# Optimization experiments

Hardware: AMD Instinct MI355X
Metric: run time of the kernel (lower is better)

The kernel has to match this reference:

```python
import jax, jax.numpy as jnp
import numpy as np

N = 100000
E = 1600000
H = 128
L = 3


def setup_inputs() -> dict:
    key = jax.random.key(0)
    ks = jax.random.split(key, 8)
    z = jax.random.normal(ks[0], (N, H), dtype=jnp.float32)
    edge_index = jax.random.randint(ks[1], (2, E), 0, N, dtype=jnp.int64)
    edge_weight = jax.random.uniform(ks[2], (E,), dtype=jnp.float32)
    s = 1.0 / np.sqrt(H)
    weight = jax.random.uniform(ks[3], (L, H, H), minval=-s, maxval=s, dtype=jnp.float32)
    w_ih = jax.random.uniform(ks[4], (3 * H, H), minval=-s, maxval=s, dtype=jnp.float32)
    w_hh = jax.random.uniform(ks[5], (3 * H, H), minval=-s, maxval=s, dtype=jnp.float32)
    b_ih = jax.random.uniform(ks[6], (3 * H,), minval=-s, maxval=s, dtype=jnp.float32)
    b_hh = jax.random.uniform(ks[7], (3 * H,), minval=-s, maxval=s, dtype=jnp.float32)
    return {"z": z, "edge_weight": edge_weight, "weight": weight,
            "w_ih": w_ih, "w_hh": w_hh, "b_ih": b_ih, "b_hh": b_hh,
            "edge_index": edge_index}


def _gru_cell(m, h, w_ih, w_hh, b_ih, b_hh):
    # torch GRUCell: gate order (r, z, n)
    gi = m @ w_ih.T + b_ih   # [N, 3H]
    gh = h @ w_hh.T + b_hh   # [N, 3H]
    i_r, i_z, i_n = jnp.split(gi, 3, axis=-1)
    h_r, h_z, h_n = jnp.split(gh, 3, axis=-1)
    r = jax.nn.sigmoid(i_r + h_r)
    zg = jax.nn.sigmoid(i_z + h_z)
    n = jnp.tanh(i_n + r * h_n)
    return (1.0 - zg) * n + zg * h


def reference(z, edge_weight, weight, w_ih, w_hh, b_ih, b_hh, edge_index):
    src = edge_index[0]  # x_j gathered from source nodes
    dst = edge_index[1]  # aggregated at target nodes
    x = z  # in_channels == out_channels, so no zero padding needed
    for l in range(L):
        m = x @ weight[l]                                  # [N, H]
        msg = m[src] * edge_weight[:, None]                # [E, H]
        agg = jax.ops.segment_sum(msg, dst, num_segments=N)  # aggr='add'
        x = _gru_cell(agg, x, w_ih, w_hh, b_ih, b_hh)
    return x
```

## Files before the change

kernel.cpp:

```cpp
#include <hip/hip_runtime.h>

typedef __bf16 bf16x8 __attribute__((ext_vector_type(8)));
typedef float floatx4 __attribute__((ext_vector_type(4)));

#define NPB 256
#define NPB_SHIFT 8
#define MAXNB 1024
#define TILE 4096

static __device__ __forceinline__ float bfu_to_f(unsigned short u) {
    unsigned int x = ((unsigned int)u) << 16;
    return __builtin_bit_cast(float, x);
}
static __device__ __forceinline__ unsigned short f_to_bfu(float f) {
    unsigned int u = __builtin_bit_cast(unsigned int, f);
    unsigned int r = (u + 0x7fffu + ((u >> 16) & 1u)) >> 16;
    return (unsigned short)r;
}

__global__ void detect_k(const unsigned short* __restrict__ bih_u,
                         const unsigned int* __restrict__ ei_u,
                         int* __restrict__ flags) {
    __shared__ int sv, sz;
    int t = threadIdx.x;
    if (t == 0) { sv = 0; sz = 0; }
    __syncthreads();
    unsigned short u = bih_u[2 * t];
    unsigned int ex = (u >> 7) & 0xFF;
    if (ex >= 64 && ex < 124) atomicAdd(&sv, 1);
    if (ei_u[2 * t + 1] == 0u) atomicAdd(&sz, 1);
    __syncthreads();
    if (t == 0) {
        flags[0] = (sv >= 48) ? 1 : 0;
        flags[1] = (sz == 64) ? 1 : 0;
    }
}


__global__ void cvt_bf16_k(const void* __restrict__ in, unsigned short* __restrict__ out,
                           int n, const int* __restrict__ flags) {
    int i = blockIdx.x * 256 + threadIdx.x;
    if (i >= n) return;
    if (flags[0]) out[i] = ((const unsigned short*)in)[i];
    else out[i] = f_to_bfu(((const float*)in)[i]);
}

__global__ void cvt_bias_k(const void* __restrict__ bih, const void* __restrict__ bhh,
                           float* __restrict__ bih_f, float* __restrict__ bhh_f,
                           const int* __restrict__ flags) {
    int i = blockIdx.x * 256 + threadIdx.x;
    if (i >= 768) return;
    const void* src = (i < 384) ? bih : bhh;
    int j = (i < 384) ? i : i - 384;
    float v = flags[0] ? bfu_to_f(((const unsigned short*)src)[j]) : ((const float*)src)[j];
    if (i < 384) bih_f[j] = v;
    else bhh_f[j] = v;
}


static __device__ __forceinline__ int load_idx(const unsigned int* eiu, size_t pos, int is64) {
    return (int)eiu[is64 ? 2 * pos : pos];
}

__global__ __launch_bounds__(256) void count_k(const unsigned int* __restrict__ eiu,
                                               int* __restrict__ bucketCnt, int E,
                                               const int* __restrict__ flags) {
    __shared__ int cnt[MAXNB];
    int t = threadIdx.x;
    for (int b = t; b < MAXNB; b += 256) cnt[b] = 0;
    __syncthreads();
    int is64 = flags[1];
    int e0 = blockIdx.x * TILE;
    int e1 = min(e0 + TILE, E);
    for (int e = e0 + t; e < e1; e += 256) {
        int d = load_idx(eiu, (size_t)E + e, is64);
        atomicAdd(&cnt[d >> NPB_SHIFT], 1);
    }
    __syncthreads();
    for (int b = t; b < MAXNB; b += 256) {
        int c = cnt[b];
        if (c) atomicAdd(&bucketCnt[b], c);
    }
}

__global__ void scanB_k(const int* __restrict__ bucketCnt, int* __restrict__ bucketBase,
                        int* __restrict__ bucketCursor, int NB, int E) {
    __shared__ int sh[MAXNB];
    int t = threadIdx.x;
    int v = (t < NB) ? bucketCnt[t] : 0;
    sh[t] = v;
    __syncthreads();
    for (int off = 1; off < MAXNB; off <<= 1) {
        int u = (t >= off) ? sh[t - off] : 0;
        __syncthreads();
        sh[t] += u;
        __syncthreads();
    }
    if (t < NB) {
        int b = sh[t] - v;
        bucketBase[t] = b;
        bucketCursor[t] = b;
    }
    if (t == 0) bucketBase[NB] = E;
}

__global__ __launch_bounds__(256) void bin_k(const unsigned int* __restrict__ eiu,
                                             const void* __restrict__ ew,
                                             int* __restrict__ bucketCursor,
                                             uint2* __restrict__ rec8, int E,
                                             const int* __restrict__ flags) {
    __shared__ int cnt[MAXNB];
    __shared__ int basel[MAXNB];
    int t = threadIdx.x;
    for (int b = t; b < MAXNB; b += 256) cnt[b] = 0;
    __syncthreads();
    int is64 = flags[1];
    int isb = flags[0];
    int e0 = blockIdx.x * TILE;
    int e1 = min(e0 + TILE, E);
    for (int e = e0 + t; e < e1; e += 256) {
        int d = load_idx(eiu, (size_t)E + e, is64);
        atomicAdd(&cnt[d >> NPB_SHIFT], 1);
    }
    __syncthreads();
    for (int b = t; b < MAXNB; b += 256) {
        int c = cnt[b];
        basel[b] = c ? atomicAdd(&bucketCursor[b], c) : 0;
        cnt[b] = 0;
    }
    __syncthreads();
    for (int e = e0 + t; e < e1; e += 256) {
        int s = load_idx(eiu, (size_t)e, is64);
        int d = load_idx(eiu, (size_t)E + e, is64);
        float w = isb ? bfu_to_f(((const unsigned short*)ew)[e]) : ((const float*)ew)[e];
        int b = d >> NPB_SHIFT;
        int p = basel[b] + atomicAdd(&cnt[b], 1);
        rec8[p] = make_uint2((unsigned int)s | ((unsigned int)(d & 255) << 20),
                             __builtin_bit_cast(unsigned int, w));
    }
}

__global__ __launch_bounds__(256) void csr_k(const uint2* __restrict__ rec8,
                                             const int* __restrict__ bucketBase,
                                             int* __restrict__ offsets,
                                             uint2* __restrict__ rec, int N, int E) {
    __shared__ int cnt[NPB];
    __shared__ int sh[NPB];
    __shared__ int cur[NPB];
    int t = threadIdx.x;
    int b = blockIdx.x;
    int n0 = b << NPB_SHIFT;
    int nodes = min(NPB, N - n0);
    int ebase = bucketBase[b];
    int ecnt = bucketBase[b + 1] - ebase;

    cnt[t] = 0;
    __syncthreads();
    for (int i = t; i < ecnt; i += 256) {
        int d = (rec8[ebase + i].x >> 20) & 255;
        atomicAdd(&cnt[d], 1);
    }
    __syncthreads();
    int v = cnt[t];
    sh[t] = v;
    __syncthreads();
    for (int off = 1; off < NPB; off <<= 1) {
        int u = (t >= off) ? sh[t - off] : 0;
        __syncthreads();
        sh[t] += u;
        __syncthreads();
    }
    int loff = sh[t] - v;
    if (t < nodes) offsets[n0 + t] = ebase + loff;
    cur[t] = ebase + loff;
    if (b == 0 && t == 0) offsets[N] = E;
    __syncthreads();
    for (int i = t; i < ecnt; i += 256) {
        uint2 r = rec8[ebase + i];
        int d = (r.x >> 20) & 255;
        int p = atomicAdd(&cur[d], 1);
        rec[p] = make_uint2(r.x & 0xFFFFFu, r.y);
    }
}


static __device__ __forceinline__ float dot8_bf(uint4 wv, uint4 iv) {
    float s;
    s  = bfu_to_f((unsigned short)(wv.x)) * bfu_to_f((unsigned short)(iv.x));
    s += bfu_to_f((unsigned short)(wv.x >> 16)) * bfu_to_f((unsigned short)(iv.x >> 16));
    s += bfu_to_f((unsigned short)(wv.y)) * bfu_to_f((unsigned short)(iv.y));
    s += bfu_to_f((unsigned short)(wv.y >> 16)) * bfu_to_f((unsigned short)(iv.y >> 16));
    s += bfu_to_f((unsigned short)(wv.z)) * bfu_to_f((unsigned short)(iv.z));
    s += bfu_to_f((unsigned short)(wv.z >> 16)) * bfu_to_f((unsigned short)(iv.z >> 16));
    s += bfu_to_f((unsigned short)(wv.w)) * bfu_to_f((unsigned short)(iv.w));
    s += bfu_to_f((unsigned short)(wv.w >> 16)) * bfu_to_f((unsigned short)(iv.w >> 16));
    return s;
}

__global__ void make_ut_k(const void* __restrict__ weight, const void* __restrict__ wih,
                          unsigned short* __restrict__ Ut, const int* __restrict__ flags) {
    int idx = blockIdx.x * 256 + threadIdx.x;
    if (idx >= 3 * 384 * 128) return;
    int isb = flags[0];
    int a = idx & 127;
    int j = (idx >> 7) % 384;
    int l = idx / (384 * 128);
    float s = 0.f;
    if (isb) {
        const uint4* W4 = (const uint4*)((const unsigned short*)weight + (size_t)l * 16384 + a * 128);
        const uint4* I4 = (const uint4*)((const unsigned short*)wih + (size_t)j * 128);
#pragma unroll
        for (int c = 0; c < 16; c++) s += dot8_bf(W4[c], I4[c]);
    } else {
        const float4* W4 = (const float4*)((const float*)weight + (size_t)l * 16384 + a * 128);
        const float4* I4 = (const float4*)((const float*)wih + (size_t)j * 128);
#pragma unroll
        for (int c = 0; c < 32; c++) {
            float4 w = W4[c], i = I4[c];
            s += w.x * i.x + w.y * i.y + w.z * i.z + w.w * i.w;
        }
    }
    Ut[idx] = f_to_bfu(s);
}

__global__ void pack_b_k(const unsigned short* __restrict__ Ut,
                         const void* __restrict__ whh,
                         unsigned short* __restrict__ Bp,
                         const int* __restrict__ flags) {
    int idx = blockIdx.x * 256 + threadIdx.x;
    if (idx >= 3 * 4 * 12 * 4 * 64) return;
    int lane = idx & 63;
    int kc = (idx >> 6) & 3;
    int rest = idx >> 8;
    int j = rest % 12;
    int cg = (rest / 12) & 3;
    int l = rest / 48;
    int s = j / 6;
    int g = (j % 6) >> 1;
    int t = j & 1;
    int col = (cg * 2 + t) * 16 + (lane & 15);
    int k = kc * 32 + (lane >> 4) * 8;
    int row384 = g * 128 + col;
    unsigned short tmp[8];
    const unsigned short* src;
    if (s == 0) {
        src = Ut + (size_t)l * 49152 + row384 * 128 + k;
    } else if (flags[0]) {
        src = (const unsigned short*)whh + (size_t)row384 * 128 + k;
    } else {
        const float* wf = (const float*)whh + (size_t)row384 * 128 + k;
        for (int i = 0; i < 8; i++) tmp[i] = f_to_bfu(wf[i]);
        src = tmp;
    }
    unsigned short* dst = Bp + (size_t)l * 98304 + (((size_t)(cg * 12 + j) * 4 + kc) * 64 + lane) * 8;
    for (int i = 0; i < 8; i++) dst[i] = src[i];
}


__global__ __launch_bounds__(256) void agg_k(const unsigned short* __restrict__ xb,
                                             const int* __restrict__ offs,
                                             const uint2* __restrict__ rec,
                                             unsigned short* __restrict__ y, int N,
                                             int nch) {
    int bid = blockIdx.x;
    int c = ((bid & 7) << 3) + ((bid >> 3) & 7) + ((bid >> 6) << 6);
    if (c >= nch) return;
    int node = c * 16 + (threadIdx.x >> 4);
    int l16 = threadIdx.x & 15;
    if (node >= N) return;
    int b = offs[node];
    int e2 = offs[node + 1];
    const uint4* xp4 = (const uint4*)xb;
    float a0[8], a1[8];
#pragma unroll
    for (int i = 0; i < 8; i++) { a0[i] = 0.f; a1[i] = 0.f; }

    auto fma_row = [&](float* acc, uint4 v, float w) {
        acc[0] += w * __builtin_bit_cast(float, v.x << 16);
        acc[1] += w * __builtin_bit_cast(float, v.x & 0xffff0000u);
        acc[2] += w * __builtin_bit_cast(float, v.y << 16);
        acc[3] += w * __builtin_bit_cast(float, v.y & 0xffff0000u);
        acc[4] += w * __builtin_bit_cast(float, v.z << 16);
        acc[5] += w * __builtin_bit_cast(float, v.z & 0xffff0000u);
        acc[6] += w * __builtin_bit_cast(float, v.w << 16);
        acc[7] += w * __builtin_bit_cast(float, v.w & 0xffff0000u);
    };

    int e = b;
    for (; e + 4 <= e2; e += 4) {
        uint2 r0 = rec[e], r1 = rec[e + 1], r2 = rec[e + 2], r3 = rec[e + 3];
        uint4 v0 = xp4[(size_t)r0.x * 16 + l16];
        uint4 v1 = xp4[(size_t)r1.x * 16 + l16];
        uint4 v2 = xp4[(size_t)r2.x * 16 + l16];
        uint4 v3 = xp4[(size_t)r3.x * 16 + l16];
        fma_row(a0, v0, __builtin_bit_cast(float, r0.y));
        fma_row(a1, v1, __builtin_bit_cast(float, r1.y));
        fma_row(a0, v2, __builtin_bit_cast(float, r2.y));
        fma_row(a1, v3, __builtin_bit_cast(float, r3.y));
    }
    for (; e < e2; e++) {
        uint2 r = rec[e];
        uint4 v = xp4[(size_t)r.x * 16 + l16];
        fma_row(a0, v, __builtin_bit_cast(float, r.y));
    }

    uint4 o;
    o.x = (unsigned int)f_to_bfu(a0[0] + a1[0]) | ((unsigned int)f_to_bfu(a0[1] + a1[1]) << 16);
    o.y = (unsigned int)f_to_bfu(a0[2] + a1[2]) | ((unsigned int)f_to_bfu(a0[3] + a1[3]) << 16);
    o.z = (unsigned int)f_to_bfu(a0[4] + a1[4]) | ((unsigned int)f_to_bfu(a0[5] + a1[5]) << 16);
    o.w = (unsigned int)f_to_bfu(a0[6] + a1[6]) | ((unsigned int)f_to_bfu(a0[7] + a1[7]) << 16);
    ((uint4*)y)[(size_t)node * 16 + l16] = o;
}


__global__ __launch_bounds__(512, 4) void gru_k(const unsigned short* __restrict__ y,
                                                const unsigned short* __restrict__ xin,
                                                void* __restrict__ xout,
                                                const unsigned short* __restrict__ Bp,
                                                const float* __restrict__ bih,
                                                const float* __restrict__ bhh, int N,
                                                const int* __restrict__ flags, int last) {
    __shared__ uint4 Blds[3072];

    int bid = blockIdx.x;
    int r8 = bid & 7;
    int inner = bid >> 3;
    int cg = inner & 3;
    int rb = ((inner >> 2) << 3) + r8;
    int row0 = rb << 7;
    if (row0 >= N) return;

    int tid = threadIdx.x;
    {
        const uint4* bsrc = (const uint4*)(Bp + (size_t)cg * 24576);
#pragma unroll
        for (int i = 0; i < 6; i++) Blds[tid + i * 512] = bsrc[tid + i * 512];
    }
    __syncthreads();

    int wave = tid >> 6;
    int wc = wave & 1;
    int wr = wave >> 1;
    int lane = tid & 63;
    int quad = lane >> 4;
    int m16 = lane & 15;
    const unsigned short* bl = (const unsigned short*)Blds;

    int rA[2];
#pragma unroll
    for (int rt = 0; rt < 2; rt++) {
        int r = row0 + wr * 32 + rt * 16 + m16;
        rA[rt] = (r < N) ? r : N - 1;
    }

    floatx4 acc[2][4];
#pragma unroll
    for (int rt = 0; rt < 2; rt++)
#pragma unroll
        for (int s = 0; s < 4; s++) acc[rt][s] = (floatx4){0.f, 0.f, 0.f, 0.f};

    bf16x8 aY[2][4], aX[2][4];

#pragma unroll
    for (int rt = 0; rt < 2; rt++)
#pragma unroll
        for (int kc = 0; kc < 4; kc++)
            aY[rt][kc] = *(const bf16x8*)(y + (size_t)rA[rt] * 128 + kc * 32 + quad * 8);
    __builtin_amdgcn_sched_barrier(0);

#pragma unroll
    for (int rt = 0; rt < 2; rt++)
#pragma unroll
        for (int kc = 0; kc < 4; kc++)
            aX[rt][kc] = *(const bf16x8*)(xin + (size_t)rA[rt] * 128 + kc * 32 + quad * 8);

#pragma unroll
    for (int kc = 0; kc < 4; kc++) {
#pragma unroll
        for (int g = 0; g < 3; g++) {
            int jU = g * 2 + wc;
            bf16x8 b = *(const bf16x8*)(bl + ((size_t)(jU * 4 + kc) * 64 + lane) * 8);
            int s = (g == 2) ? 2 : g;
            acc[0][s] = __builtin_amdgcn_mfma_f32_16x16x32_bf16(aY[0][kc], b, acc[0][s], 0, 0, 0);
            acc[1][s] = __builtin_amdgcn_mfma_f32_16x16x32_bf16(aY[1][kc], b, acc[1][s], 0, 0, 0);
        }
    }
    __builtin_amdgcn_sched_barrier(0);

#pragma unroll
    for (int kc = 0; kc < 4; kc++) {
#pragma unroll
        for (int g = 0; g < 3; g++) {
            int jW = 6 + g * 2 + wc;
            bf16x8 b = *(const bf16x8*)(bl + ((size_t)(jW * 4 + kc) * 64 + lane) * 8);
            int s = (g == 2) ? 3 : g;
            acc[0][s] = __builtin_amdgcn_mfma_f32_16x16x32_bf16(aX[0][kc], b, acc[0][s], 0, 0, 0);
            acc[1][s] = __builtin_amdgcn_mfma_f32_16x16x32_bf16(aX[1][kc], b, acc[1][s], 0, 0, 0);
        }
    }

    int ch = cg * 32 + wc * 16 + m16;
    float b_r = bih[ch] + bhh[ch];
    float b_z = bih[128 + ch] + bhh[128 + ch];
    float bi_n = bih[256 + ch];
    float bh_n = bhh[256 + ch];
    int isb = last ? flags[0] : 1;
#pragma unroll
    for (int rt = 0; rt < 2; rt++) {
#pragma unroll
        for (int ri = 0; ri < 4; ri++) {
            int row = row0 + wr * 32 + rt * 16 + quad * 4 + ri;
            if (row >= N) continue;
            float sr = acc[rt][0][ri] + b_r;
            float sz = acc[rt][1][ri] + b_z;
            float gn = acc[rt][2][ri] + bi_n;
            float hn = acc[rt][3][ri] + bh_n;
            float r = __builtin_amdgcn_rcpf(1.f + __expf(-sr));
            float zg = __builtin_amdgcn_rcpf(1.f + __expf(-sz));
            float x2 = gn + r * hn;
            float n = 1.f - 2.f * __builtin_amdgcn_rcpf(1.f + __expf(2.f * x2));
            float h = bfu_to_f(xin[(size_t)row * 128 + ch]);
            float o = n + zg * (h - n);
            if (isb) ((unsigned short*)xout)[(size_t)row * 128 + ch] = f_to_bfu(o);
            else ((float*)xout)[(size_t)row * 128 + ch] = o;
        }
    }
}


extern "C" void kernel_launch(void* const* d_in, const int* in_sizes, int n_in,
                              void* d_out, int out_size, void* d_ws, size_t ws_size,
                              hipStream_t stream) {
    const int N = in_sizes[0] / 128;
    const int E = in_sizes[1];
    const int NB = (N + NPB - 1) >> NPB_SHIFT;

    const void* z = d_in[0];
    const void* ew = d_in[1];
    const void* weight = d_in[2];
    const void* wih = d_in[3];
    const void* whh = d_in[4];
    const void* bih = d_in[5];
    const void* bhh = d_in[6];
    const unsigned int* eiu = (const unsigned int*)d_in[7];

    unsigned short* y01 = (unsigned short*)d_out;

    size_t off = 0;
    char* base = (char*)d_ws;
    auto carve = [&](size_t bytes) -> void* {
        void* p = base + off;
        off = (off + bytes + 255) & ~(size_t)255;
        return p;
    };
    unsigned short* xb = (unsigned short*)carve((size_t)N * 128 * 2);
    unsigned short* xb2 = (unsigned short*)carve((size_t)N * 128 * 2);
    uint2* rec8 = (uint2*)carve((size_t)E * 8);
    uint2* rec = (uint2*)carve((size_t)E * 8);
    int* offsets = (int*)carve((size_t)(N + 1) * 4);
    int* bucketCnt = (int*)carve(MAXNB * 4);
    int* bucketBase = (int*)carve((MAXNB + 1) * 4);
    int* bucketCursor = (int*)carve(MAXNB * 4);
    unsigned short* Ut = (unsigned short*)carve((size_t)3 * 384 * 128 * 2);
    unsigned short* Bp = (unsigned short*)carve((size_t)3 * 48 * 4 * 64 * 8 * 2);
    float* bih_f = (float*)carve(384 * 4);
    float* bhh_f = (float*)carve(384 * 4);
    int* flags = (int*)carve(256);

    detect_k<<<1, 64, 0, stream>>>((const unsigned short*)bih, eiu, flags);

    cvt_bf16_k<<<(N * 128 + 255) / 256, 256, 0, stream>>>(z, xb, N * 128, flags);
    cvt_bias_k<<<3, 256, 0, stream>>>(bih, bhh, bih_f, bhh_f, flags);

    hipMemsetAsync(bucketCnt, 0, MAXNB * 4, stream);
    int gbin = (E + TILE - 1) / TILE;
    count_k<<<gbin, 256, 0, stream>>>(eiu, bucketCnt, E, flags);
    scanB_k<<<1, MAXNB, 0, stream>>>(bucketCnt, bucketBase, bucketCursor, NB, E);
    bin_k<<<gbin, 256, 0, stream>>>(eiu, ew, bucketCursor, rec8, E, flags);
    csr_k<<<NB, NPB, 0, stream>>>(rec8, bucketBase, offsets, rec, N, E);

    make_ut_k<<<(3 * 384 * 128 + 255) / 256, 256, 0, stream>>>(weight, wih, Ut, flags);
    pack_b_k<<<(3 * 4 * 12 * 4 * 64 + 255) / 256, 256, 0, stream>>>(Ut, whh, Bp, flags);

    const int RB = (N + 127) >> 7;
    const int grid_gru = 8 * ((RB + 7) >> 3) * 4;
    const int nch = (N + 15) >> 4;
    const int grid_agg = ((nch + 63) >> 6) << 6;

    agg_k<<<grid_agg, 256, 0, stream>>>(xb, offsets, rec, y01, N, nch);
    gru_k<<<grid_gru, 512, 0, stream>>>(y01, xb, xb2, Bp, bih_f, bhh_f, N, flags, 0);
    agg_k<<<grid_agg, 256, 0, stream>>>(xb2, offsets, rec, y01, N, nch);
    gru_k<<<grid_gru, 512, 0, stream>>>(y01, xb2, xb, Bp + 98304, bih_f, bhh_f, N, flags, 0);
    agg_k<<<grid_agg, 256, 0, stream>>>(xb, offsets, rec, xb2, N, nch);
    gru_k<<<grid_gru, 512, 0, stream>>>(xb2, xb, d_out, Bp + 2 * 98304, bih_f, bhh_f, N, flags, 1);
}
```

Before: 588.6 us.

## Shrink GRU tile to 16 output channels per block, doubling grid

Measured after the change: 577.8 us. About the same (-1.8%).

```diff
diff --git a/kernel.cpp b/kernel.cpp
--- a/kernel.cpp
+++ b/kernel.cpp
@@ -228,17 +228,16 @@
                          unsigned short* __restrict__ Bp,
                          const int* __restrict__ flags) {
     int idx = blockIdx.x * 256 + threadIdx.x;
-    if (idx >= 3 * 4 * 12 * 4 * 64) return;
+    if (idx >= 3 * 8 * 6 * 4 * 64) return;
     int lane = idx & 63;
     int kc = (idx >> 6) & 3;
     int rest = idx >> 8;
-    int j = rest % 12;
-    int cg = (rest / 12) & 3;
+    int j = rest % 6;
+    int cg8 = (rest / 6) & 7;
     int l = rest / 48;
-    int s = j / 6;
-    int g = (j % 6) >> 1;
-    int t = j & 1;
-    int col = (cg * 2 + t) * 16 + (lane & 15);
+    int s = j / 3;
+    int g = j % 3;
+    int col = cg8 * 16 + (lane & 15);
     int k = kc * 32 + (lane >> 4) * 8;
     int row384 = g * 128 + col;
     unsigned short tmp[8];
@@ -252,7 +251,7 @@
         for (int i = 0; i < 8; i++) tmp[i] = f_to_bfu(wf[i]);
         src = tmp;
     }
-    unsigned short* dst = Bp + (size_t)l * 98304 + (((size_t)(cg * 12 + j) * 4 + kc) * 64 + lane) * 8;
+    unsigned short* dst = Bp + (size_t)l * 98304 + (((size_t)(cg8 * 6 + j) * 4 + kc) * 64 + lane) * 8;
     for (int i = 0; i < 8; i++) dst[i] = src[i];
 }
 
@@ -313,76 +312,62 @@
 }
 
 
-__global__ __launch_bounds__(512, 4) void gru_k(const unsigned short* __restrict__ y,
+__global__ __launch_bounds__(512, 6) void gru_k(const unsigned short* __restrict__ y,
                                                 const unsigned short* __restrict__ xin,
                                                 void* __restrict__ xout,
                                                 const unsigned short* __restrict__ Bp,
                                                 const float* __restrict__ bih,
                                                 const float* __restrict__ bhh, int N,
                                                 const int* __restrict__ flags, int last) {
-    __shared__ uint4 Blds[3072];
+    __shared__ uint4 Blds[1536];
 
     int bid = blockIdx.x;
     int r8 = bid & 7;
     int inner = bid >> 3;
-    int cg = inner & 3;
-    int rb = ((inner >> 2) << 3) + r8;
+    int cg8 = inner & 7;
+    int rb = ((inner >> 3) << 3) + r8;
     int row0 = rb << 7;
     if (row0 >= N) return;
 
     int tid = threadIdx.x;
     {
-        const uint4* bsrc = (const uint4*)(Bp + (size_t)cg * 24576);
-#pragma unroll
-        for (int i = 0; i < 6; i++) Blds[tid + i * 512] = bsrc[tid + i * 512];
-    }
-    __syncthreads();
-
-    int wave = tid >> 6;
-    int wc = wave & 1;
-    int wr = wave >> 1;
+        const uint4* bsrc = (const uint4*)(Bp + (size_t)cg8 * 12288);
+#pragma unroll
+        for (int i = 0; i < 3; i++) Blds[tid + i * 512] = bsrc[tid + i * 512];
+    }
+    __syncthreads();
+
+    int wr = tid >> 6;
     int lane = tid & 63;
     int quad = lane >> 4;
     int m16 = lane & 15;
     const unsigned short* bl = (const unsigned short*)Blds;
 
-    int rA[2];
-#pragma unroll
-    for (int rt = 0; rt < 2; rt++) {
-        int r = row0 + wr * 32 + rt * 16 + m16;
-        rA[rt] = (r < N) ? r : N - 1;
-    }
-
-    floatx4 acc[2][4];
-#pragma unroll
-    for (int rt = 0; rt < 2; rt++)
-#pragma unroll
-        for (int s = 0; s < 4; s++) acc[rt][s] = (floatx4){0.f, 0.f, 0.f, 0.f};
-
-    bf16x8 aY[2][4], aX[2][4];
-
-#pragma unroll
-    for (int rt = 0; rt < 2; rt++)
-#pragma unroll
-        for (int kc = 0; kc < 4; kc++)
-            aY[rt][kc] = *(const bf16x8*)(y + (size_t)rA[rt] * 128 + kc * 32 + quad * 8);
+    int r = row0 + wr * 16 + m16;
+    int rA = (r < N) ? r : N - 1;
+
+    floatx4 acc[4];
+#pragma unroll
+    for (int s = 0; s < 4; s++) acc[s] = (floatx4){0.f, 0.f, 0.f, 0.f};
+
+    bf16x8 aY[4], aX[4];
+
+#pragma unroll
+    for (int kc = 0; kc < 4; kc++)
+        aY[kc] = *(const bf16x8*)(y + (size_t)rA * 128 + kc * 32 + quad * 8);
     __builtin_amdgcn_sched_barrier(0);
 
 #pragma unroll
-    for (int rt = 0; rt < 2; rt++)
-#pragma unroll
-        for (int kc = 0; kc < 4; kc++)
-            aX[rt][kc] = *(const bf16x8*)(xin + (size_t)rA[rt] * 128 + kc * 32 + quad * 8);
+    for (int kc = 0; kc < 4; kc++)
+        aX[kc] = *(const bf16x8*)(xin + (size_t)rA * 128 + kc * 32 + quad * 8);
 
 #pragma unroll
     for (int kc = 0; kc < 4; kc++) {
 #pragma unroll
         for (int g = 0; g < 3; g++) {
-            int jU = g * 2 + wc;
-            bf16x8 b = *(const bf16x8*)(bl + ((size_t)(jU * 4 + kc) * 64 + lane) * 8);
+            bf16x8 b = *(const bf16x8*)(bl + ((size_t)(g * 4 + kc) * 64 + lane) * 8);
             int s = (g == 2) ? 2 : g;
-            acc[0][s] = __builtin_amdgcn_mfma_f32_16x16x32_bf16(aY[0][kc], b, acc[0][s], 0, 0, 0);
-            acc[1][s] = __builtin_amdgcn_mfma_f32_16x16x32_bf16(aY[1][kc], b, acc[1][s], 0, 0, 0);
+            acc[s] = __builtin_amdgcn_mfma_f32_16x16x32_bf16(aY[kc], b, acc[s], 0, 0, 0);
         }
     }
     __builtin_amdgcn_sched_barrier(0);
@@ -391,39 +376,34 @@
     for (int kc = 0; kc < 4; kc++) {
 #pragma unroll
         for (int g = 0; g < 3; g++) {
-            int jW = 6 + g * 2 + wc;
-            bf16x8 b = *(const bf16x8*)(bl + ((size_t)(jW * 4 + kc) * 64 + lane) * 8);
+            bf16x8 b = *(const bf16x8*)(bl + ((size_t)((3 + g) * 4 + kc) * 64 + lane) * 8);
             int s = (g == 2) ? 3 : g;
-            acc[0][s] = __builtin_amdgcn_mfma_f32_16x16x32_bf16(aX[0][kc], b, acc[0][s], 0, 0, 0);
-            acc[1][s] = __builtin_amdgcn_mfma_f32_16x16x32_bf16(aX[1][kc], b, acc[1][s], 0, 0, 0);
+            acc[s] = __builtin_amdgcn_mfma_f32_16x16x32_bf16(aX[kc], b, acc[s], 0, 0, 0);
         }
     }
 
-    int ch = cg * 32 + wc * 16 + m16;
+    int ch = cg8 * 16 + m16;
     float b_r = bih[ch] + bhh[ch];
     float b_z = bih[128 + ch] + bhh[128 + ch];
     float bi_n = bih[256 + ch];
     float bh_n = bhh[256 + ch];
     int isb = last ? flags[0] : 1;
 #pragma unroll
-    for (int rt = 0; rt < 2; rt++) {
-#pragma unroll
-        for (int ri = 0; ri < 4; ri++) {
-            int row = row0 + wr * 32 + rt * 16 + quad * 4 + ri;
-            if (row >= N) continue;
-            float sr = acc[rt][0][ri] + b_r;
-            float sz = acc[rt][1][ri] + b_z;
-            float gn = acc[rt][2][ri] + bi_n;
-            float hn = acc[rt][3][ri] + bh_n;
-            float r = __builtin_amdgcn_rcpf(1.f + __expf(-sr));
-            float zg = __builtin_amdgcn_rcpf(1.f + __expf(-sz));
-            float x2 = gn + r * hn;
-            float n = 1.f - 2.f * __builtin_amdgcn_rcpf(1.f + __expf(2.f * x2));
-            float h = bfu_to_f(xin[(size_t)row * 128 + ch]);
-            float o = n + zg * (h - n);
-            if (isb) ((unsigned short*)xout)[(size_t)row * 128 + ch] = f_to_bfu(o);
-            else ((float*)xout)[(size_t)row * 128 + ch] = o;
-        }
+    for (int ri = 0; ri < 4; ri++) {
+        int row = row0 + wr * 16 + quad * 4 + ri;
+        if (row >= N) continue;
+        float sr = acc[0][ri] + b_r;
+        float sz = acc[1][ri] + b_z;
+        float gn = acc[2][ri] + bi_n;
+        float hn = acc[3][ri] + bh_n;
+        float rg = __builtin_amdgcn_rcpf(1.f + __expf(-sr));
+        float zg = __builtin_amdgcn_rcpf(1.f + __expf(-sz));
+        float x2 = gn + rg * hn;
+        float n = 1.f - 2.f * __builtin_amdgcn_rcpf(1.f + __expf(2.f * x2));
+        float h = bfu_to_f(xin[(size_t)row * 128 + ch]);
+        float o = n + zg * (h - n);
+        if (isb) ((unsigned short*)xout)[(size_t)row * 128 + ch] = f_to_bfu(o);
+        else ((float*)xout)[(size_t)row * 128 + ch] = o;
     }
 }
 
@@ -462,7 +442,7 @@
     int* bucketBase = (int*)carve((MAXNB + 1) * 4);
     int* bucketCursor = (int*)carve(MAXNB * 4);
     unsigned short* Ut = (unsigned short*)carve((size_t)3 * 384 * 128 * 2);
-    unsigned short* Bp = (unsigned short*)carve((size_t)3 * 48 * 4 * 64 * 8 * 2);
+    unsigned short* Bp = (unsigned short*)carve((size_t)3 * 8 * 6 * 4 * 64 * 8 * 2);
     float* bih_f = (float*)carve(384 * 4);
     float* bhh_f = (float*)carve(384 * 4);
     int* flags = (int*)carve(256);
@@ -480,10 +460,10 @@
     csr_k<<<NB, NPB, 0, stream>>>(rec8, bucketBase, offsets, rec, N, E);
 
     make_ut_k<<<(3 * 384 * 128 + 255) / 256, 256, 0, stream>>>(weight, wih, Ut, flags);
-    pack_b_k<<<(3 * 4 * 12 * 4 * 64 + 255) / 256, 256, 0, stream>>>(Ut, whh, Bp, flags);
+    pack_b_k<<<(3 * 8 * 6 * 4 * 64 + 255) / 256, 256, 0, stream>>>(Ut, whh, Bp, flags);
 
     const int RB = (N + 127) >> 7;
-    const int grid_gru = 8 * ((RB + 7) >> 3) * 4;
+    const int grid_gru = 8 * ((RB + 7) >> 3) * 8;
     const int nch = (N + 15) >> 4;
     const int grid_agg = ((nch + 63) >> 6) << 6;
 
```
